# Kernel optimization log

Hardware: AMD Instinct MI355X
Metric: run time of the kernel (lower is better)

## Reference

```python
import jax, jax.numpy as jnp
import numpy as np

N, E = 50000, 800000
NFEAT, NHID = 128, 128


def setup_inputs() -> dict:
    key = jax.random.key(0)
    ks = jax.random.split(key, 10)
    s = 1.0 / np.sqrt(NFEAT)
    inp = {
        "x": jax.random.normal(ks[0], (N, NFEAT), dtype=jnp.float32),
        "edge_index": jax.random.randint(ks[1], (2, E), 0, N, dtype=jnp.int32),
        "head": 0,
        # Relation params (nn.Linear weights, [out, in], bias=False)
        "gamma1_w": jax.random.uniform(ks[2], (NFEAT, NFEAT), jnp.float32, -s, s),
        "gamma2_w": jax.random.uniform(ks[3], (NFEAT, NFEAT), jnp.float32, -s, s),
        "beta1_w": jax.random.uniform(ks[4], (NFEAT, NFEAT), jnp.float32, -s, s),
        "beta2_w": jax.random.uniform(ks[5], (NFEAT, NFEAT), jnp.float32, -s, s),
        "r": jax.random.uniform(ks[6], (1, NFEAT), jnp.float32, -s, s),
        # GCNConv params: lin (bias=False) + conv bias
        "lin_w": jax.random.uniform(ks[7], (NHID, NFEAT), jnp.float32, -s, s),
        "bias": jnp.zeros((NHID,), dtype=jnp.float32),
    }
    return inp


def _lrelu(v):
    return jnp.where(v >= 0, v, 0.2 * v)  # LeakyReLU(0.2)


def _forward(x, edge_index, gamma1_w, gamma2_w, beta1_w, beta2_w, r, lin_w, bias):
    n = x.shape[0]
    row, col = edge_index[0], edge_index[1]
    ones_e = jnp.ones((edge_index.shape[1],), dtype=x.dtype)

    # num_neighbor = scatter_add(ones, row); neighbor = scatter_mean(x[col], row)
    num_neighbor = jax.ops.segment_sum(ones_e, row, num_segments=n)  # [N]
    neigh_sum = jax.ops.segment_sum(x[col], row, num_segments=n)      # [N, F]
    neighbor = neigh_sum / jnp.maximum(num_neighbor, 1.0)[:, None]

    # Relation (ablation=0): FiLM-style translation vector
    gamma = _lrelu(x @ gamma1_w.T + neighbor @ gamma2_w.T) + 1.0
    beta = _lrelu(x @ beta1_w.T + neighbor @ beta2_w.T)
    output = x + (gamma * r + beta) - neighbor                        # [N, F]

    xw = x @ lin_w.T                                                  # [N, H]
    loop = jnp.arange(n, dtype=row.dtype)
    row2 = jnp.concatenate([row, loop])
    col2 = jnp.concatenate([col, loop])
    deg = jax.ops.segment_sum(jnp.ones_like(row2, dtype=x.dtype), col2, num_segments=n)
    dinv = jnp.where(deg > 0, jax.lax.rsqrt(deg), 0.0)
    norm = dinv[row2] * dinv[col2]                                    # [E+N]
    h_k = jax.ops.segment_sum(norm[:, None] * xw[row2], col2, num_segments=n) + bias

    # tail branch (head=False, ablation=0): h_s = output, projected by gc.lin.weight
    h_s = output @ lin_w.T
    h_k = (h_k + h_s) / (num_neighbor + 1.0)[:, None]
    return h_k, output


def reference(x, edge_index, head, gamma1_w, gamma2_w, beta1_w, beta2_w, r, lin_w, bias):
    # head is a static Python int (0 -> tail branch, the full fused path)
    assert not head
    return _forward(x, edge_index, gamma1_w, gamma2_w, beta1_w, beta2_w, r, lin_w, bias)
```

## Files before the change

kernel.cpp:

```cpp
#include <hip/hip_runtime.h>

#define NN 50000
#define NE 800000
#define NF 128
#define QS (NN * 32)

#define SHIFT 8
#define NB 196
#define PBLOCKS 128
#define PCHUNK ((NE + PBLOCKS - 1) / PBLOCKS)

#define NTILES ((NN + 63) / 64)
#define FBLOCKS 512

#define CVX_BLOCKS 3125
#define CVW_BLOCKS 320
#define PREP_BLOCKS (CVX_BLOCKS + CVW_BLOCKS + PBLOCKS)

typedef __attribute__((ext_vector_type(4))) float f32x4;
typedef __attribute__((ext_vector_type(8))) short bf16x8;

__device__ __forceinline__ short f2bf(float f) {
    unsigned u = __float_as_uint(f);
    u += 0x7FFF + ((u >> 16) & 1);
    return (short)(u >> 16);
}
__device__ __forceinline__ float bf2f(short s) {
    return __uint_as_float(((unsigned)(unsigned short)s) << 16);
}

__global__ __launch_bounds__(256) void prep_kernel(
    const float* __restrict__ x, const float* __restrict__ g1,
    const float* __restrict__ g2, const float* __restrict__ b1,
    const float* __restrict__ b2, const float* __restrict__ lin,
    const int* __restrict__ ei, short* __restrict__ xq,
    short* __restrict__ wbf, int* __restrict__ gcnt) {
    __shared__ int cnt[2 * NB];
    int bid = blockIdx.x;
    int t = threadIdx.x;

    if (bid < CVX_BLOCKS) {
        int i = bid * 256 + t;
        if (i < NN * 16) {
            int n = i >> 4, c = i & 15;
            int q = c >> 2, sub = c & 3;
            float4 a = ((const float4*)x)[i * 2];
            float4 b = ((const float4*)x)[i * 2 + 1];
            bf16x8 v;
            v[0] = f2bf(a.x); v[1] = f2bf(a.y); v[2] = f2bf(a.z); v[3] = f2bf(a.w);
            v[4] = f2bf(b.x); v[5] = f2bf(b.y); v[6] = f2bf(b.z); v[7] = f2bf(b.w);
            *(bf16x8*)(xq + (size_t)q * QS + n * 32 + sub * 8) = v;
        }
        return;
    }
    if (bid < CVX_BLOCKS + CVW_BLOCKS) {
        int i = (bid - CVX_BLOCKS) * 256 + t;
        if (i < 5 * NF * NF) {
            int m = i >> 14, off = i & (NF * NF - 1);
            float v = (m == 0) ? g1[off] : (m == 1) ? g2[off] : (m == 2) ? b1[off]
                    : (m == 3) ? b2[off] : lin[off];
            wbf[i] = f2bf(v);
        }
        return;
    }
    int pb = bid - CVX_BLOCKS - CVW_BLOCKS;
    for (int i = t; i < 2 * NB; i += 256) cnt[i] = 0;
    __syncthreads();
    int lo = pb * PCHUNK;
    int hi = min(lo + PCHUNK, NE);
    for (int j = lo + t; j < hi; j += 256) {
        int r = ei[j];
        int c = ei[NE + j];
        atomicAdd(&cnt[r >> SHIFT], 1);
        atomicAdd(&cnt[NB + (c >> SHIFT)], 1);
    }
    __syncthreads();
    for (int i = t; i < 2 * NB; i += 256)
        if (cnt[i]) atomicAdd(&gcnt[i], cnt[i]);
}

__global__ __launch_bounds__(256) void p1_scan_kernel(const int* __restrict__ gcnt,
                                                      int* __restrict__ baseR,
                                                      int* __restrict__ baseC,
                                                      int* __restrict__ gcur) {
    __shared__ int s[256];
    int t = threadIdx.x;
    int v = (t < NB) ? gcnt[t] : 0;
    s[t] = v;
    __syncthreads();
    for (int off = 1; off < 256; off <<= 1) {
        int u = (t >= off) ? s[t - off] : 0;
        __syncthreads();
        s[t] += u;
        __syncthreads();
    }
    if (t < NB) {
        int excl = s[t] - v;
        baseR[t] = excl;
        gcur[t] = excl;
        if (t == NB - 1) baseR[NB] = s[t];
    }
    __syncthreads();
    int v2 = (t < NB) ? gcnt[NB + t] : 0;
    s[t] = v2;
    __syncthreads();
    for (int off = 1; off < 256; off <<= 1) {
        int u = (t >= off) ? s[t - off] : 0;
        __syncthreads();
        s[t] += u;
        __syncthreads();
    }
    if (t < NB) {
        int excl = s[t] - v2;
        baseC[t] = excl;
        gcur[NB + t] = excl;
        if (t == NB - 1) baseC[NB] = s[t];
    }
}

__global__ __launch_bounds__(256) void p2_partition_kernel(const int* __restrict__ ei,
                                                           int* __restrict__ gcur,
                                                           unsigned* __restrict__ partR,
                                                           unsigned* __restrict__ partC) {
    __shared__ int cnt[2 * NB];
    __shared__ int res[2 * NB];
    int t = threadIdx.x;
    for (int i = t; i < 2 * NB; i += 256) cnt[i] = 0;
    __syncthreads();
    int lo = blockIdx.x * PCHUNK;
    int hi = min(lo + PCHUNK, NE);
    for (int j = lo + t; j < hi; j += 256) {
        int r = ei[j];
        int c = ei[NE + j];
        atomicAdd(&cnt[r >> SHIFT], 1);
        atomicAdd(&cnt[NB + (c >> SHIFT)], 1);
    }
    __syncthreads();
    for (int i = t; i < 2 * NB; i += 256) {
        int n = cnt[i];
        res[i] = n ? atomicAdd(&gcur[i], n) : 0;
        cnt[i] = 0;
    }
    __syncthreads();
    for (int j = lo + t; j < hi; j += 256) {
        int r = ei[j];
        int c = ei[NE + j];
        int bR = r >> SHIFT;
        int sR = atomicAdd(&cnt[bR], 1);
        partR[res[bR] + sR] = ((unsigned)(r & 255) << 17) | (unsigned)c;
        int bC = NB + (c >> SHIFT);
        int sC = atomicAdd(&cnt[bC], 1);
        partC[res[bC] + sC] = ((unsigned)(c & 255) << 17) | (unsigned)r;
    }
}

__global__ __launch_bounds__(256) void p3_build_kernel(
    const unsigned* __restrict__ partR, const unsigned* __restrict__ partC,
    const int* __restrict__ baseR, const int* __restrict__ baseC,
    int* __restrict__ offs_r, int* __restrict__ offs_c,
    int* __restrict__ csr_r, int* __restrict__ csr_c,
    int* __restrict__ degr, float* __restrict__ dinv) {
    int side = blockIdx.x / NB;
    int b = blockIdx.x - side * NB;
    const unsigned* part = side ? partC : partR;
    const int* base = side ? baseC : baseR;
    int* offs = side ? offs_c : offs_r;
    int* csr = side ? csr_c : csr_r;

    __shared__ int deg[256];
    __shared__ int cur[256];
    int t = threadIdx.x;
    int s0 = base[b], s1 = base[b + 1];
    deg[t] = 0;
    __syncthreads();
    for (int j = s0 + t; j < s1; j += 256)
        atomicAdd(&deg[part[j] >> 17], 1);
    __syncthreads();
    int myDeg = deg[t];
    for (int off = 1; off < 256; off <<= 1) {
        int u = (t >= off) ? deg[t - off] : 0;
        __syncthreads();
        deg[t] += u;
        __syncthreads();
    }
    int excl = deg[t] - myDeg;
    int node = (b << SHIFT) + t;
    if (node <= NN) offs[node] = s0 + excl;
    if (node < NN) {
        if (side == 0) degr[node] = myDeg;
        else           dinv[node] = rsqrtf((float)myDeg + 1.0f);
    }
    cur[t] = excl;
    __syncthreads();
    for (int j = s0 + t; j < s1; j += 256) {
        unsigned en = part[j];
        int k = en >> 17;
        int p = atomicAdd(&cur[k], 1);
        csr[s0 + p] = (int)(en & 0x1FFFFu);
    }
}

__global__ __launch_bounds__(256) void gather_fused_kernel(
    const int* __restrict__ offs_r, const int* __restrict__ csr_r,
    const int* __restrict__ offs_c, const int* __restrict__ csr_c,
    const short* __restrict__ xq, const float* __restrict__ dinv,
    short* __restrict__ nbq, short* __restrict__ zq) {
    int q = blockIdx.x & 3;
    int grp = blockIdx.x >> 2;
    int t = threadIdx.x;
    int g = grp * 16 + (t >> 4);
    int slot = (t >> 2) & 3;
    int fl = t & 3;
    const short* xb = xq + (size_t)q * QS + fl * 8;

    int s = offs_r[g], e = offs_r[g + 1];
    float acc[8] = {0.f, 0.f, 0.f, 0.f, 0.f, 0.f, 0.f, 0.f};
    int j = s + slot;
    for (; j + 4 < e; j += 8) {
        int s0 = csr_r[j], s1 = csr_r[j + 4];
        bf16x8 v0 = *(const bf16x8*)(xb + s0 * 32);
        bf16x8 v1 = *(const bf16x8*)(xb + s1 * 32);
        #pragma unroll
        for (int k = 0; k < 8; ++k) acc[k] += bf2f(v0[k]) + bf2f(v1[k]);
    }
    for (; j < e; j += 4) {
        bf16x8 v = *(const bf16x8*)(xb + csr_r[j] * 32);
        #pragma unroll
        for (int k = 0; k < 8; ++k) acc[k] += bf2f(v[k]);
    }
    #pragma unroll
    for (int k = 0; k < 8; ++k) {
        acc[k] += __shfl_xor(acc[k], 4);
        acc[k] += __shfl_xor(acc[k], 8);
    }
    if (slot == 0) {
        float invn = 1.0f / fmaxf((float)(e - s), 1.0f);
        bf16x8 o;
        #pragma unroll
        for (int k = 0; k < 8; ++k) o[k] = f2bf(acc[k] * invn);
        *(bf16x8*)(nbq + (size_t)q * QS + g * 32 + fl * 8) = o;
    }

    s = offs_c[g]; e = offs_c[g + 1];
    float az[8] = {0.f, 0.f, 0.f, 0.f, 0.f, 0.f, 0.f, 0.f};
    j = s + slot;
    for (; j + 4 < e; j += 8) {
        int s0 = csr_c[j], s1 = csr_c[j + 4];
        float w0 = dinv[s0], w1 = dinv[s1];
        bf16x8 v0 = *(const bf16x8*)(xb + s0 * 32);
        bf16x8 v1 = *(const bf16x8*)(xb + s1 * 32);
        #pragma unroll
        for (int k = 0; k < 8; ++k) az[k] += w0 * bf2f(v0[k]) + w1 * bf2f(v1[k]);
    }
    for (; j < e; j += 4) {
        int s0 = csr_c[j];
        float w0 = dinv[s0];
        bf16x8 v = *(const bf16x8*)(xb + s0 * 32);
        #pragma unroll
        for (int k = 0; k < 8; ++k) az[k] += w0 * bf2f(v[k]);
    }
    #pragma unroll
    for (int k = 0; k < 8; ++k) {
        az[k] += __shfl_xor(az[k], 4);
        az[k] += __shfl_xor(az[k], 8);
    }
    if (slot == 0) {
        float dc = dinv[g];
        bf16x8 self = *(const bf16x8*)(xb + g * 32);
        bf16x8 zo;
        #pragma unroll
        for (int k = 0; k < 8; ++k) zo[k] = f2bf(dc * (az[k] + dc * bf2f(self[k])));
        *(bf16x8*)(zq + (size_t)q * QS + g * 32 + fl * 8) = zo;
    }
}

__global__ __launch_bounds__(256, 2) void film_mfma_kernel(
    const short* __restrict__ xq, const short* __restrict__ nbq,
    const short* __restrict__ zq, const short* __restrict__ wbf,
    const float* __restrict__ rvec, const float* __restrict__ bias,
    const int* __restrict__ degr, float* __restrict__ outp,
    float* __restrict__ hko) {
    __shared__ short xs[64 * NF];
    __shared__ short ns[64 * NF];
    __shared__ short zs[64 * NF];

    int tid = threadIdx.x;
    int w = tid >> 6;
    int l = tid & 63;
    int lr = l & 15;
    int lg = l >> 4;

    bf16x8 wf[2][5][4];
    float rc[2], bc[2];
    #pragma unroll
    for (int j = 0; j < 2; ++j) {
        int col = (2 * w + j) * 16 + lr;
        #pragma unroll
        for (int m = 0; m < 5; ++m) {
            const short* wm = wbf + m * 16384 + col * NF;
            #pragma unroll
            for (int kb = 0; kb < 4; ++kb)
                wf[j][m][kb] = *(const bf16x8*)(wm + kb * 32 + lg * 8);
        }
        rc[j] = rvec[col];
        bc[j] = bias[col];
    }

    #pragma unroll 1
    for (int tile = blockIdx.x; tile < NTILES; tile += FBLOCKS) {
        int node0 = tile * 64;

        #pragma unroll
        for (int it = 0; it < 4; ++it) {
            int chunk = it * 256 + tid;
            int row = chunk >> 4;
            int c = chunk & 15;
            int grow = min(node0 + row, NN - 1);
            int swz = ((c ^ (row & 7)) << 3);
            size_t qoff = (size_t)(c >> 2) * QS + grow * 32 + (c & 3) * 8;
            *(bf16x8*)(xs + row * NF + swz) = *(const bf16x8*)(xq + qoff);
            *(bf16x8*)(ns + row * NF + swz) = *(const bf16x8*)(nbq + qoff);
            *(bf16x8*)(zs + row * NF + swz) = *(const bf16x8*)(zq + qoff);
        }
        __syncthreads();

        #pragma unroll 1
        for (int rg = 0; rg < 4; ++rg) {
            bf16x8 xf[4], nf[4];
            #pragma unroll
            for (int kb = 0; kb < 4; ++kb) {
                int row = rg * 16 + lr;
                int swz = (((kb * 4 + lg) ^ (row & 7)) << 3);
                xf[kb] = *(const bf16x8*)(xs + row * NF + swz);
                nf[kb] = *(const bf16x8*)(ns + row * NF + swz);
            }
            #pragma unroll
            for (int j = 0; j < 2; ++j) {
                f32x4 ag = {0.f, 0.f, 0.f, 0.f};
                f32x4 ab = {0.f, 0.f, 0.f, 0.f};
                #pragma unroll
                for (int kb = 0; kb < 4; ++kb) {
                    ag = __builtin_amdgcn_mfma_f32_16x16x32_bf16(xf[kb], wf[j][0][kb], ag, 0, 0, 0);
                    ag = __builtin_amdgcn_mfma_f32_16x16x32_bf16(nf[kb], wf[j][1][kb], ag, 0, 0, 0);
                    ab = __builtin_amdgcn_mfma_f32_16x16x32_bf16(xf[kb], wf[j][2][kb], ab, 0, 0, 0);
                    ab = __builtin_amdgcn_mfma_f32_16x16x32_bf16(nf[kb], wf[j][3][kb], ab, 0, 0, 0);
                }
                int col = (2 * w + j) * 16 + lr;
                #pragma unroll
                for (int q = 0; q < 4; ++q) {
                    int nl = rg * 16 + lg * 4 + q;
                    int ng = node0 + nl;
                    int addr = nl * NF + (((col >> 3) ^ (nl & 7)) << 3) + (col & 7);
                    float xv = bf2f(xs[addr]);
                    float nv = bf2f(ns[addr]);
                    float gp = ag[q], bp = ab[q];
                    float gamma = (gp >= 0.f ? gp : 0.2f * gp) + 1.0f;
                    float beta  = (bp >= 0.f ? bp : 0.2f * bp);
                    float o = xv + gamma * rc[j] + beta - nv;
                    if (ng < NN) outp[ng * NF + col] = o;
                    zs[addr] = f2bf(o + bf2f(zs[addr]));
                }
            }
        }
        __syncthreads();

        #pragma unroll 1
        for (int rg = 0; rg < 4; ++rg) {
            bf16x8 of[4];
            #pragma unroll
            for (int kb = 0; kb < 4; ++kb) {
                int row = rg * 16 + lr;
                int swz = (((kb * 4 + lg) ^ (row & 7)) << 3);
                of[kb] = *(const bf16x8*)(zs + row * NF + swz);
            }
            float invdq[4];
            #pragma unroll
            for (int q = 0; q < 4; ++q)
                invdq[q] = 1.0f / ((float)degr[min(node0 + rg * 16 + lg * 4 + q, NN - 1)] + 1.0f);
            #pragma unroll
            for (int j = 0; j < 2; ++j) {
                f32x4 as = {0.f, 0.f, 0.f, 0.f};
                #pragma unroll
                for (int kb = 0; kb < 4; ++kb)
                    as = __builtin_amdgcn_mfma_f32_16x16x32_bf16(of[kb], wf[j][4][kb], as, 0, 0, 0);
                int col = (2 * w + j) * 16 + lr;
                #pragma unroll
                for (int q = 0; q < 4; ++q) {
                    int ng = node0 + rg * 16 + lg * 4 + q;
                    if (ng < NN) hko[ng * NF + col] = (as[q] + bc[j]) * invdq[q];
                }
            }
        }
        __syncthreads();
    }
}

extern "C" void kernel_launch(void* const* d_in, const int* in_sizes, int n_in,
                              void* d_out, int out_size, void* d_ws, size_t ws_size,
                              hipStream_t stream) {
    const float* x    = (const float*)d_in[0];
    const int*   ei   = (const int*)d_in[1];
    const float* g1   = (const float*)d_in[3];
    const float* g2   = (const float*)d_in[4];
    const float* b1   = (const float*)d_in[5];
    const float* b2   = (const float*)d_in[6];
    const float* rv   = (const float*)d_in[7];
    const float* lin  = (const float*)d_in[8];
    const float* bias = (const float*)d_in[9];

    float* dinv = (float*)d_ws;
    int* degr   = (int*)(dinv + NN);
    int* offs_r = degr + NN;
    int* offs_c = offs_r + (NN + 1);
    int* csr_r  = offs_c + (NN + 1);
    int* csr_c  = csr_r + NE;
    unsigned* partR = (unsigned*)(csr_c + NE);
    unsigned* partC = partR + NE;
    int* gcnt   = (int*)(partC + NE);
    int* gcur   = gcnt + 2 * NB;
    int* baseR  = gcur + 2 * NB;
    int* baseC  = baseR + (NB + 1);
    uintptr_t p = (uintptr_t)(baseC + NB + 1);
    p = (p + 15) & ~(uintptr_t)15;
    short* xq   = (short*)p;
    short* nbq  = xq + 4 * QS;
    short* zq   = nbq + 4 * QS;
    short* wbf  = zq + 4 * QS;

    float* hko  = (float*)d_out;
    float* outp = hko + NN * NF;

    hipMemsetAsync(gcnt, 0, 2 * NB * sizeof(int), stream);

    prep_kernel<<<PREP_BLOCKS, 256, 0, stream>>>(x, g1, g2, b1, b2, lin, ei,
                                                 xq, wbf, gcnt);
    p1_scan_kernel<<<1, 256, 0, stream>>>(gcnt, baseR, baseC, gcur);
    p2_partition_kernel<<<PBLOCKS, 256, 0, stream>>>(ei, gcur, partR, partC);
    p3_build_kernel<<<2 * NB, 256, 0, stream>>>(partR, partC, baseR, baseC,
                                                offs_r, offs_c, csr_r, csr_c, degr, dinv);
    gather_fused_kernel<<<(NN / 16) * 4, 256, 0, stream>>>(offs_r, csr_r, offs_c, csr_c,
                                                           xq, dinv, nbq, zq);
    film_mfma_kernel<<<FBLOCKS, 256, 0, stream>>>(xq, nbq, zq, wbf, rv, bias, degr,
                                                  outp, hko);
}
```

Before: 172.5 us.

## Prescale x by dinv and run both gathers concurrently in split thread halves

The CSR build kernel now writes a dinv-scaled bf16 copy of x, so the GCN gather no longer loads dinv per edge. The gather kernel splits each node's 16 threads into two halves that run the mean-neighbour gather and the normalized GCN gather at the same time instead of one after the other. Column indices are read as int2 pairs, with extra handling for odd start and end positions. The cost is an extra scaled-x buffer written and read, an additional bf16 rounding of dinv*x, and only two edge slots per half instead of four.

```diff
diff --git a/kernel.cpp b/kernel.cpp
--- a/kernel.cpp
+++ b/kernel.cpp
@@ -159,7 +159,8 @@
     const int* __restrict__ baseR, const int* __restrict__ baseC,
     int* __restrict__ offs_r, int* __restrict__ offs_c,
     int* __restrict__ csr_r, int* __restrict__ csr_c,
-    int* __restrict__ degr, float* __restrict__ dinv) {
+    int* __restrict__ degr, float* __restrict__ dinv,
+    const short* __restrict__ xq, short* __restrict__ xdq) {
     int side = blockIdx.x / NB;
     int b = blockIdx.x - side * NB;
     const unsigned* part = side ? partC : partR;
@@ -169,6 +170,7 @@
 
     __shared__ int deg[256];
     __shared__ int cur[256];
+    __shared__ float dinvs[256];
     int t = threadIdx.x;
     int s0 = base[b], s1 = base[b + 1];
     deg[t] = 0;
@@ -188,7 +190,11 @@
     if (node <= NN) offs[node] = s0 + excl;
     if (node < NN) {
         if (side == 0) degr[node] = myDeg;
-        else           dinv[node] = rsqrtf((float)myDeg + 1.0f);
+        else {
+            float dc = rsqrtf((float)myDeg + 1.0f);
+            dinv[node] = dc;
+            dinvs[t] = dc;
+        }
     }
     cur[t] = excl;
     __syncthreads();
@@ -198,79 +204,101 @@
         int p = atomicAdd(&cur[k], 1);
         csr[s0 + p] = (int)(en & 0x1FFFFu);
     }
+    if (side == 1) {
+        #pragma unroll 1
+        for (int pass = 0; pass < 4; ++pass) {
+            int nl = pass * 64 + (t >> 2);
+            int ci = t & 3;
+            int node2 = (b << SHIFT) + nl;
+            if (node2 < NN) {
+                float dc = dinvs[nl];
+                #pragma unroll
+                for (int qi = 0; qi < 4; ++qi) {
+                    bf16x8 v = *(const bf16x8*)(xq + (size_t)qi * QS + node2 * 32 + ci * 8);
+                    bf16x8 o;
+                    #pragma unroll
+                    for (int k = 0; k < 8; ++k) o[k] = f2bf(dc * bf2f(v[k]));
+                    *(bf16x8*)(xdq + (size_t)qi * QS + node2 * 32 + ci * 8) = o;
+                }
+            }
+        }
+    }
 }
 
 __global__ __launch_bounds__(256) void gather_fused_kernel(
     const int* __restrict__ offs_r, const int* __restrict__ csr_r,
     const int* __restrict__ offs_c, const int* __restrict__ csr_c,
-    const short* __restrict__ xq, const float* __restrict__ dinv,
+    const short* __restrict__ xq, const short* __restrict__ xdq,
+    const float* __restrict__ dinv,
     short* __restrict__ nbq, short* __restrict__ zq) {
     int q = blockIdx.x & 3;
     int grp = blockIdx.x >> 2;
     int t = threadIdx.x;
     int g = grp * 16 + (t >> 4);
-    int slot = (t >> 2) & 3;
+    int half = (t >> 3) & 1;
+    int ps = (t >> 2) & 1;
     int fl = t & 3;
-    const short* xb = xq + (size_t)q * QS + fl * 8;
-
-    int s = offs_r[g], e = offs_r[g + 1];
+
+    const short* xb = (half ? xdq : xq) + (size_t)q * QS + fl * 8;
+    const int* offs = half ? offs_c : offs_r;
+    const int* csr  = half ? csr_c  : csr_r;
+
+    int s = offs[g], e = offs[g + 1];
+    int deg = e - s;
+
     float acc[8] = {0.f, 0.f, 0.f, 0.f, 0.f, 0.f, 0.f, 0.f};
-    int j = s + slot;
-    for (; j + 4 < e; j += 8) {
-        int s0 = csr_r[j], s1 = csr_r[j + 4];
-        bf16x8 v0 = *(const bf16x8*)(xb + s0 * 32);
-        bf16x8 v1 = *(const bf16x8*)(xb + s1 * 32);
+
+    if (s & 1) {
+        if (ps == 0) {
+            bf16x8 v = *(const bf16x8*)(xb + csr[s] * 32);
+            #pragma unroll
+            for (int k = 0; k < 8; ++k) acc[k] += bf2f(v[k]);
+        }
+        ++s;
+    }
+    int npairs = (e - s) >> 1;
+    int p = ps;
+    for (; p + 2 < npairs; p += 4) {
+        int2 c0 = *(const int2*)(csr + s + 2 * p);
+        int2 c1 = *(const int2*)(csr + s + 2 * p + 4);
+        bf16x8 v0 = *(const bf16x8*)(xb + c0.x * 32);
+        bf16x8 v1 = *(const bf16x8*)(xb + c0.y * 32);
+        bf16x8 v2 = *(const bf16x8*)(xb + c1.x * 32);
+        bf16x8 v3 = *(const bf16x8*)(xb + c1.y * 32);
+        #pragma unroll
+        for (int k = 0; k < 8; ++k)
+            acc[k] += (bf2f(v0[k]) + bf2f(v1[k])) + (bf2f(v2[k]) + bf2f(v3[k]));
+    }
+    for (; p < npairs; p += 2) {
+        int2 c0 = *(const int2*)(csr + s + 2 * p);
+        bf16x8 v0 = *(const bf16x8*)(xb + c0.x * 32);
+        bf16x8 v1 = *(const bf16x8*)(xb + c0.y * 32);
         #pragma unroll
         for (int k = 0; k < 8; ++k) acc[k] += bf2f(v0[k]) + bf2f(v1[k]);
     }
-    for (; j < e; j += 4) {
-        bf16x8 v = *(const bf16x8*)(xb + csr_r[j] * 32);
+    if (((e - s) & 1) && ps == 0) {
+        bf16x8 v = *(const bf16x8*)(xb + csr[e - 1] * 32);
         #pragma unroll
         for (int k = 0; k < 8; ++k) acc[k] += bf2f(v[k]);
     }
     #pragma unroll
-    for (int k = 0; k < 8; ++k) {
-        acc[k] += __shfl_xor(acc[k], 4);
-        acc[k] += __shfl_xor(acc[k], 8);
-    }
-    if (slot == 0) {
-        float invn = 1.0f / fmaxf((float)(e - s), 1.0f);
-        bf16x8 o;
-        #pragma unroll
-        for (int k = 0; k < 8; ++k) o[k] = f2bf(acc[k] * invn);
-        *(bf16x8*)(nbq + (size_t)q * QS + g * 32 + fl * 8) = o;
-    }
-
-    s = offs_c[g]; e = offs_c[g + 1];
-    float az[8] = {0.f, 0.f, 0.f, 0.f, 0.f, 0.f, 0.f, 0.f};
-    j = s + slot;
-    for (; j + 4 < e; j += 8) {
-        int s0 = csr_c[j], s1 = csr_c[j + 4];
-        float w0 = dinv[s0], w1 = dinv[s1];
-        bf16x8 v0 = *(const bf16x8*)(xb + s0 * 32);
-        bf16x8 v1 = *(const bf16x8*)(xb + s1 * 32);
-        #pragma unroll
-        for (int k = 0; k < 8; ++k) az[k] += w0 * bf2f(v0[k]) + w1 * bf2f(v1[k]);
-    }
-    for (; j < e; j += 4) {
-        int s0 = csr_c[j];
-        float w0 = dinv[s0];
-        bf16x8 v = *(const bf16x8*)(xb + s0 * 32);
-        #pragma unroll
-        for (int k = 0; k < 8; ++k) az[k] += w0 * bf2f(v[k]);
-    }
-    #pragma unroll
-    for (int k = 0; k < 8; ++k) {
-        az[k] += __shfl_xor(az[k], 4);
-        az[k] += __shfl_xor(az[k], 8);
-    }
-    if (slot == 0) {
-        float dc = dinv[g];
-        bf16x8 self = *(const bf16x8*)(xb + g * 32);
-        bf16x8 zo;
-        #pragma unroll
-        for (int k = 0; k < 8; ++k) zo[k] = f2bf(dc * (az[k] + dc * bf2f(self[k])));
-        *(bf16x8*)(zq + (size_t)q * QS + g * 32 + fl * 8) = zo;
+    for (int k = 0; k < 8; ++k) acc[k] += __shfl_xor(acc[k], 4);
+
+    if (ps == 0) {
+        if (half == 0) {
+            float invn = 1.0f / fmaxf((float)deg, 1.0f);
+            bf16x8 o;
+            #pragma unroll
+            for (int k = 0; k < 8; ++k) o[k] = f2bf(acc[k] * invn);
+            *(bf16x8*)(nbq + (size_t)q * QS + g * 32 + fl * 8) = o;
+        } else {
+            float dc = dinv[g];
+            bf16x8 self = *(const bf16x8*)(xb + g * 32);
+            bf16x8 zo;
+            #pragma unroll
+            for (int k = 0; k < 8; ++k) zo[k] = f2bf(dc * (acc[k] + bf2f(self[k])));
+            *(bf16x8*)(zq + (size_t)q * QS + g * 32 + fl * 8) = zo;
+        }
     }
 }
 
@@ -411,8 +439,8 @@
     float* dinv = (float*)d_ws;
     int* degr   = (int*)(dinv + NN);
     int* offs_r = degr + NN;
-    int* offs_c = offs_r + (NN + 1);
-    int* csr_r  = offs_c + (NN + 1);
+    int* offs_c = offs_r + (NN + 2);
+    int* csr_r  = offs_c + (NN + 2);
     int* csr_c  = csr_r + NE;
     unsigned* partR = (unsigned*)(csr_c + NE);
     unsigned* partC = partR + NE;
@@ -425,7 +453,8 @@
     short* xq   = (short*)p;
     short* nbq  = xq + 4 * QS;
     short* zq   = nbq + 4 * QS;
-    short* wbf  = zq + 4 * QS;
+    short* xdq  = zq + 4 * QS;
+    short* wbf  = xdq + 4 * QS;
 
     float* hko  = (float*)d_out;
     float* outp = hko + NN * NF;
@@ -437,9 +466,10 @@
     p1_scan_kernel<<<1, 256, 0, stream>>>(gcnt, baseR, baseC, gcur);
     p2_partition_kernel<<<PBLOCKS, 256, 0, stream>>>(ei, gcur, partR, partC);
     p3_build_kernel<<<2 * NB, 256, 0, stream>>>(partR, partC, baseR, baseC,
-                                                offs_r, offs_c, csr_r, csr_c, degr, dinv);
+                                                offs_r, offs_c, csr_r, csr_c,
+                                                degr, dinv, xq, xdq);
     gather_fused_kernel<<<(NN / 16) * 4, 256, 0, stream>>>(offs_r, csr_r, offs_c, csr_c,
-                                                           xq, dinv, nbq, zq);
+                                                           xq, xdq, dinv, nbq, zq);
     film_mfma_kernel<<<FBLOCKS, 256, 0, stream>>>(xq, nbq, zq, wbf, rv, bias, degr,
                                                   outp, hko);
 }
```

Result: faster. 168.3 us (median of 2 runs) (-2.4%).
